# Optimization experiments

Measured on AMD Instinct MI355X. Metric: run time of the kernel, lower is better.

## Reference

```python
import jax, jax.numpy as jnp
import numpy as np

B, C, H, W = 4, 128, 64, 64
NUM_HEADS = 4
HEAD_DIM = C // NUM_HEADS


def setup_inputs() -> dict:
    key = jax.random.key(0)
    ks = jax.random.split(key, 9)
    s = 0.02
    return {
        "x": jax.random.normal(ks[0], (B, C, H, W), dtype=jnp.float32),
        "wq": jax.random.normal(ks[1], (C, C), dtype=jnp.float32) * s,
        "bq": jax.random.normal(ks[2], (C,), dtype=jnp.float32) * s,
        "wk": jax.random.normal(ks[3], (C, C), dtype=jnp.float32) * s,
        "bk": jax.random.normal(ks[4], (C,), dtype=jnp.float32) * s,
        "wv": jax.random.normal(ks[5], (C, C), dtype=jnp.float32) * s,
        "bv": jax.random.normal(ks[6], (C,), dtype=jnp.float32) * s,
        "wo": jax.random.normal(ks[7], (C, C), dtype=jnp.float32) * s,
        "bo": jax.random.normal(ks[8], (C,), dtype=jnp.float32) * s,
    }


def _proj(w, b, xf):
    # 1x1 conv == channel-mixing linear: xf is (B, C, N)
    return jnp.einsum("oc,bcn->bon", w, xf) + b[None, :, None]


def reference(x, wq, bq, wk, bk, wv, bv, wo, bo):
    b, c, h, w = x.shape
    n = h * w
    nh, hd = NUM_HEADS, HEAD_DIM
    xf = x.reshape(b, c, n)
    q = _proj(wq, bq, xf).reshape(b, nh, hd, n)
    k = _proj(wk, bk, xf).reshape(b, nh, hd, n)
    v = _proj(wv, bv, xf).reshape(b, nh, hd, n)
    # scores: (b, heads, n, n)
    scores = jnp.einsum("bhdn,bhdm->bhnm", q, k) / jnp.sqrt(jnp.float32(hd)).astype(x.dtype)
    prob = jax.nn.softmax(scores, axis=-1)
    # attn_out: (b, heads, head_dim, n)
    attn = jnp.einsum("bhnm,bhdm->bhdn", prob, v).reshape(b, c, n)
    out = _proj(wo, bo, attn).reshape(b, c, h, w)
    return x + out
```

## Files before the change

kernel.cpp:

```cpp
#include <hip/hip_runtime.h>
#include <hip/hip_bf16.h>

#define BB 4
#define CC 128
#define NN 4096
#define NHEAD 4
#define HDIM 32
#define KSPLIT 2

typedef short bf16x8_t __attribute__((ext_vector_type(8)));
typedef float f32x4_t __attribute__((ext_vector_type(4)));
typedef int i32x4_t __attribute__((ext_vector_type(4)));

#define MFMA16(a, b, c) __builtin_amdgcn_mfma_f32_16x16x32_bf16(a, b, c, 0, 0, 0)
#define EXP2(x) __builtin_amdgcn_exp2f(x)

#define QSCALE (0.17677669529663687f * 1.4426950408889634f)

static __device__ inline unsigned short f2bf(float f) {
  unsigned u = __builtin_bit_cast(unsigned, f);
  u += 0x7fffu + ((u >> 16) & 1u);
  return (unsigned short)(u >> 16);
}
static __device__ inline unsigned pack_trunc(float lo, float hi) {
  return __builtin_amdgcn_perm(__builtin_bit_cast(unsigned, hi),
                               __builtin_bit_cast(unsigned, lo), 0x07060302u);
}

static __device__ inline void gload_lds16(const unsigned short* gsrc, void* ldst) {
  __builtin_amdgcn_global_load_lds(
      (const __attribute__((address_space(1))) unsigned int*)gsrc,
      (__attribute__((address_space(3))) unsigned int*)ldst, 16, 0, 0);
}

__global__ __launch_bounds__(256) void wconv_kernel(
    const float* __restrict__ wq, const float* __restrict__ wk,
    const float* __restrict__ wv, const float* __restrict__ wo,
    unsigned short* __restrict__ wb) {
  int f = (blockIdx.x * 256 + threadIdx.x) * 8;
  int m = f >> 14, off = f & 16383;
  const float* src = (m == 0) ? wq : (m == 1) ? wk : (m == 2) ? wv : wo;
  float sc = (m == 0) ? QSCALE : 1.0f;
  float4 a = *(const float4*)(src + off);
  float4 b = *(const float4*)(src + off + 4);
  ushort4 u0, u1;
  u0.x = f2bf(a.x * sc); u0.y = f2bf(a.y * sc); u0.z = f2bf(a.z * sc); u0.w = f2bf(a.w * sc);
  u1.x = f2bf(b.x * sc); u1.y = f2bf(b.y * sc); u1.z = f2bf(b.z * sc); u1.w = f2bf(b.w * sc);
  *(ushort4*)(wb + f) = u0;
  *(ushort4*)(wb + f + 4) = u1;
}

__global__ __launch_bounds__(256) void qkv_mfma_kernel(
    const float* __restrict__ x,
    const unsigned short* __restrict__ wqb, const unsigned short* __restrict__ wkb,
    const unsigned short* __restrict__ wvb,
    const float* __restrict__ bq, const float* __restrict__ bk,
    const float* __restrict__ bv,
    unsigned short* __restrict__ qt, unsigned short* __restrict__ kt,
    unsigned short* __restrict__ vg) {
  __shared__ float xs[CC][65];
  const int b = blockIdx.y, nt = blockIdx.x, proj = blockIdx.z;
  const int tid = threadIdx.x;

#pragma unroll
  for (int i = 0; i < 8; i++) {
    int f = tid + 256 * i;
    int c = f >> 4, n4 = (f & 15) * 4;
    float4 v4 = *(const float4*)(x + ((size_t)b * CC + c) * NN + nt * 64 + n4);
    xs[c][n4 + 0] = v4.x; xs[c][n4 + 1] = v4.y;
    xs[c][n4 + 2] = v4.z; xs[c][n4 + 3] = v4.w;
  }
  __syncthreads();

  const int lane = tid & 63, w = tid >> 6;
  const int l16 = lane & 15, g = lane >> 4;
  const int nl = w * 16;

  bf16x8_t xf[4];
#pragma unroll
  for (int ks = 0; ks < 4; ks++) {
    i32x4_t pi;
#pragma unroll
    for (int p = 0; p < 4; p++) {
      float e0 = xs[ks * 32 + g * 8 + 2 * p][nl + l16];
      float e1 = xs[ks * 32 + g * 8 + 2 * p + 1][nl + l16];
      pi[p] = (int)((unsigned)f2bf(e0) | ((unsigned)f2bf(e1) << 16));
    }
    xf[ks] = __builtin_bit_cast(bf16x8_t, pi);
  }

  const int ngl = nt * 64 + nl;

  if (proj < 2) {
    const unsigned short* wm = proj ? wkb : wqb;
    const float* bias = proj ? bk : bq;
    unsigned short* dst = proj ? kt : qt;
    float bsc = proj ? 1.0f : QSCALE;
#pragma unroll
    for (int dt = 0; dt < 8; dt++) {
      float bini = bias[dt * 16 + l16] * bsc;
      f32x4_t acc = {bini, bini, bini, bini};
#pragma unroll
      for (int ks = 0; ks < 4; ks++) {
        bf16x8_t wf = *(const bf16x8_t*)(wm + (size_t)(dt * 16 + l16) * CC + ks * 32 + g * 8);
        acc = MFMA16(xf[ks], wf, acc);
      }
      int h = dt >> 1, dcol = (dt & 1) * 16 + l16;
#pragma unroll
      for (int r = 0; r < 4; r++) {
        size_t addr = (((size_t)b * NHEAD + h) * NN + (ngl + g * 4 + r)) * HDIM + dcol;
        dst[addr] = f2bf(acc[r]);
      }
    }
  } else {
    const int n = ngl + l16;
    const int mt = n >> 6, fv = (n >> 5) & 1, g2 = (n >> 2) & 3;
    const int elem = ((n >> 4) & 1) * 4 + (n & 3);
#pragma unroll
    for (int ot = 0; ot < 8; ot++) {
      f32x4_t acc;
#pragma unroll
      for (int r = 0; r < 4; r++) acc[r] = bv[ot * 16 + g * 4 + r];
#pragma unroll
      for (int ks = 0; ks < 4; ks++) {
        bf16x8_t wf = *(const bf16x8_t*)(wvb + (size_t)(ot * 16 + l16) * CC + ks * 32 + g * 8);
        acc = MFMA16(wf, xf[ks], acc);
      }
      const int hh = ot >> 1, half = ot & 1;
      const size_t base = (((size_t)(b * NHEAD + hh) * 64 + mt) * 256) * 8;
#pragma unroll
      for (int r = 0; r < 4; r++) {
        int l16v = g * 4 + r;
        size_t idx = base + (size_t)(((fv * 2 + half) * 16 + l16v) * 4 + g2) * 8 + elem;
        vg[idx] = f2bf(acc[r]);
      }
    }
  }
}

__global__ __launch_bounds__(256, 4) void attn_mfma5_kernel(
    const unsigned short* __restrict__ qt, const unsigned short* __restrict__ kt,
    const unsigned short* __restrict__ vg,
    float* __restrict__ opart, float* __restrict__ lpart) {
  __shared__ __attribute__((aligned(16))) unsigned short smem[2][4096];

  const int chunk = blockIdx.x & (KSPLIT - 1), nt = blockIdx.x / KSPLIT;
  const int h = blockIdx.y, b = blockIdx.z;
  const int bh = b * NHEAD + h;
  const int tid = threadIdx.x, lane = tid & 63, wid = tid >> 6;
  const int l16 = lane & 15, g = lane >> 4;
  const int nbase = nt * 128 + wid * 32;

  const unsigned short* qb = qt + (size_t)bh * NN * HDIM;
  const unsigned short* kb = kt + (size_t)bh * NN * HDIM;
  const unsigned short* vgb = vg + (size_t)bh * 64 * 2048;

  const bf16x8_t qf0 = *(const bf16x8_t*)(qb + (size_t)(nbase + l16) * HDIM + g * 8);
  const bf16x8_t qf1 = *(const bf16x8_t*)(qb + (size_t)(nbase + 16 + l16) * HDIM + g * 8);

  f32x4_t o00 = {0, 0, 0, 0}, o01 = {0, 0, 0, 0};
  f32x4_t o10 = {0, 0, 0, 0}, o11 = {0, 0, 0, 0};
  f32x4_t la = {0, 0, 0, 0}, lb = {0, 0, 0, 0};
  const f32x4_t zf = {0, 0, 0, 0};
  const i32x4_t onesi = {0x3F803F80, 0x3F803F80, 0x3F803F80, 0x3F803F80};
  const bf16x8_t ones = __builtin_bit_cast(bf16x8_t, onesi);

  const int NITER = 64 / KSPLIT;
  const int mt0 = chunk * NITER;

  const unsigned short* ksrc = kb + ((size_t)mt0 * 64 + wid * 16 + l16) * HDIM + g * 8;
  const unsigned short* vsrc = vgb + (size_t)mt0 * 2048 + (size_t)((wid * 16 + l16) * 4 + g) * 8;

  auto stage = [&](int p, int i) {
    gload_lds16(ksrc + (size_t)i * 2048, &smem[p][wid * 512]);
    gload_lds16(vsrc + (size_t)i * 2048, &smem[p][2048 + wid * 512]);
  };

  auto body = [&](int p) {
    const unsigned short* sk = &smem[p][0];
    bf16x8_t k0 = *(const bf16x8_t*)(sk + 0 * 512 + lane * 8);
    bf16x8_t k1 = *(const bf16x8_t*)(sk + 1 * 512 + lane * 8);
    bf16x8_t k2 = *(const bf16x8_t*)(sk + 2 * 512 + lane * 8);
    bf16x8_t k3 = *(const bf16x8_t*)(sk + 3 * 512 + lane * 8);
    bf16x8_t vf0 = *(const bf16x8_t*)(sk + 2048 + 0 * 512 + lane * 8);
    bf16x8_t vf2 = *(const bf16x8_t*)(sk + 2048 + 1 * 512 + lane * 8);
    bf16x8_t vf1 = *(const bf16x8_t*)(sk + 2048 + 2 * 512 + lane * 8);
    bf16x8_t vf3 = *(const bf16x8_t*)(sk + 2048 + 3 * 512 + lane * 8);

    f32x4_t sA0 = MFMA16(k0, qf0, zf), sA1 = MFMA16(k1, qf0, zf);
    f32x4_t sA2 = MFMA16(k2, qf0, zf), sA3 = MFMA16(k3, qf0, zf);
    f32x4_t sB0 = MFMA16(k0, qf1, zf), sB1 = MFMA16(k1, qf1, zf);
    f32x4_t sB2 = MFMA16(k2, qf1, zf), sB3 = MFMA16(k3, qf1, zf);

#pragma unroll
    for (int r = 0; r < 4; r++) {
      sA0[r] = EXP2(sA0[r]); sA1[r] = EXP2(sA1[r]);
      sA2[r] = EXP2(sA2[r]); sA3[r] = EXP2(sA3[r]);
      sB0[r] = EXP2(sB0[r]); sB1[r] = EXP2(sB1[r]);
      sB2[r] = EXP2(sB2[r]); sB3[r] = EXP2(sB3[r]);
    }

    i32x4_t pA0i = {(int)pack_trunc(sA0[0], sA0[1]), (int)pack_trunc(sA0[2], sA0[3]),
                    (int)pack_trunc(sA1[0], sA1[1]), (int)pack_trunc(sA1[2], sA1[3])};
    i32x4_t pA1i = {(int)pack_trunc(sA2[0], sA2[1]), (int)pack_trunc(sA2[2], sA2[3]),
                    (int)pack_trunc(sA3[0], sA3[1]), (int)pack_trunc(sA3[2], sA3[3])};
    i32x4_t pB0i = {(int)pack_trunc(sB0[0], sB0[1]), (int)pack_trunc(sB0[2], sB0[3]),
                    (int)pack_trunc(sB1[0], sB1[1]), (int)pack_trunc(sB1[2], sB1[3])};
    i32x4_t pB1i = {(int)pack_trunc(sB2[0], sB2[1]), (int)pack_trunc(sB2[2], sB2[3]),
                    (int)pack_trunc(sB3[0], sB3[1]), (int)pack_trunc(sB3[2], sB3[3])};
    bf16x8_t pA0 = __builtin_bit_cast(bf16x8_t, pA0i);
    bf16x8_t pA1 = __builtin_bit_cast(bf16x8_t, pA1i);
    bf16x8_t pB0 = __builtin_bit_cast(bf16x8_t, pB0i);
    bf16x8_t pB1 = __builtin_bit_cast(bf16x8_t, pB1i);

    o00 = MFMA16(vf0, pA0, o00); o00 = MFMA16(vf1, pA1, o00);
    o01 = MFMA16(vf2, pA0, o01); o01 = MFMA16(vf3, pA1, o01);
    o10 = MFMA16(vf0, pB0, o10); o10 = MFMA16(vf1, pB1, o10);
    o11 = MFMA16(vf2, pB0, o11); o11 = MFMA16(vf3, pB1, o11);

    la = MFMA16(ones, pA0, la); la = MFMA16(ones, pA1, la);
    lb = MFMA16(ones, pB0, lb); lb = MFMA16(ones, pB1, lb);
  };

  stage(0, 0);
  __syncthreads();
  for (int mi = 0; mi < NITER; mi += 2) {
    stage(1, mi + 1);
    body(0);
    __syncthreads();
    if (mi + 2 < NITER) stage(0, mi + 2);
    body(1);
    __syncthreads();
  }

  float* obase = opart + ((size_t)(chunk * BB * NHEAD + bh)) * HDIM * NN;
#pragma unroll
  for (int r = 0; r < 4; r++) {
    obase[(size_t)(g * 4 + r) * NN + nbase + l16] = o00[r];
    obase[(size_t)(16 + g * 4 + r) * NN + nbase + l16] = o01[r];
    obase[(size_t)(g * 4 + r) * NN + nbase + 16 + l16] = o10[r];
    obase[(size_t)(16 + g * 4 + r) * NN + nbase + 16 + l16] = o11[r];
  }
  if (g == 0) {
    float* lb_ = lpart + (size_t)(chunk * BB * NHEAD + bh) * NN;
    lb_[nbase + l16] = la[0];
    lb_[nbase + 16 + l16] = lb[0];
  }
}

__global__ __launch_bounds__(256) void combine_kernel(
    const float* __restrict__ opart, const float* __restrict__ lpart,
    unsigned short* __restrict__ attnT) {
  const int n = blockIdx.x * 256 + threadIdx.x;
  const int bh = blockIdx.y, dg = blockIdx.z;
  const int b = bh >> 2, h = bh & 3;

  float l = 0.f;
#pragma unroll
  for (int c = 0; c < KSPLIT; c++) l += lpart[(size_t)(c * BB * NHEAD + bh) * NN + n];
  float inv = 1.f / l;

  unsigned dw[4];
#pragma unroll
  for (int p = 0; p < 4; p++) {
    float s0 = 0.f, s1 = 0.f;
#pragma unroll
    for (int c = 0; c < KSPLIT; c++) {
      const float* ob = opart + ((size_t)(c * BB * NHEAD + bh) * HDIM + dg * 8) * NN;
      s0 += ob[(size_t)(2 * p) * NN + n];
      s1 += ob[(size_t)(2 * p + 1) * NN + n];
    }
    dw[p] = (unsigned)f2bf(s0 * inv) | ((unsigned)f2bf(s1 * inv) << 16);
  }
  unsigned short* dst = attnT + ((size_t)b * NN + n) * CC + h * HDIM + dg * 8;
  *(uint4*)dst = *(uint4*)&dw[0];
}

__global__ __launch_bounds__(256) void out_mfma_kernel(
    const unsigned short* __restrict__ attnT, const unsigned short* __restrict__ wob,
    const float* __restrict__ bo, const float* __restrict__ x,
    float* __restrict__ out) {
  const int b = blockIdx.y, nt = blockIdx.x, half = blockIdx.z;
  const int tid = threadIdx.x, lane = tid & 63, w = tid >> 6;
  const int l16 = lane & 15, g = lane >> 4;
  const int n0 = nt * 64 + w * 16;

  bf16x8_t bf[4];
#pragma unroll
  for (int ks = 0; ks < 4; ks++)
    bf[ks] = *(const bf16x8_t*)(attnT + ((size_t)b * NN + n0 + l16) * CC + ks * 32 + g * 8);

#pragma unroll
  for (int mi = 0; mi < 4; mi++) {
    int mt = half * 4 + mi;
    f32x4_t acc;
#pragma unroll
    for (int r = 0; r < 4; r++) acc[r] = bo[mt * 16 + g * 4 + r];
#pragma unroll
    for (int ks = 0; ks < 4; ks++) {
      bf16x8_t af = *(const bf16x8_t*)(wob + (size_t)(mt * 16 + l16) * CC + ks * 32 + g * 8);
      acc = MFMA16(af, bf[ks], acc);
    }
#pragma unroll
    for (int r = 0; r < 4; r++) {
      int o = mt * 16 + g * 4 + r;
      size_t addr = ((size_t)b * CC + o) * NN + n0 + l16;
      out[addr] = acc[r] + x[addr];
    }
  }
}

extern "C" void kernel_launch(void* const* d_in, const int* in_sizes, int n_in,
                              void* d_out, int out_size, void* d_ws, size_t ws_size,
                              hipStream_t stream) {
  const float* x  = (const float*)d_in[0];
  const float* wq = (const float*)d_in[1];
  const float* bq = (const float*)d_in[2];
  const float* wk = (const float*)d_in[3];
  const float* bk = (const float*)d_in[4];
  const float* wv = (const float*)d_in[5];
  const float* bv = (const float*)d_in[6];
  const float* wo = (const float*)d_in[7];
  const float* bo = (const float*)d_in[8];
  float* out = (float*)d_out;

  char* w = (char*)d_ws;
  const size_t SZ = (size_t)BB * NHEAD * NN * HDIM * 2;
  unsigned short* qt    = (unsigned short*)w;
  unsigned short* kt    = (unsigned short*)(w + SZ);
  unsigned short* vg    = (unsigned short*)(w + 2 * SZ);
  unsigned short* wb    = (unsigned short*)(w + 3 * SZ);
  float* opart = (float*)(w + 3 * SZ + 131072);
  float* lpart = (float*)(w + 3 * SZ + 131072 +
                          (size_t)KSPLIT * BB * NHEAD * HDIM * NN * 4);
  unsigned short* attnT = qt;
  unsigned short* wqb = wb, *wkb = wb + 16384, *wvb = wb + 32768, *wob = wb + 49152;

  wconv_kernel<<<32, 256, 0, stream>>>(wq, wk, wv, wo, wb);
  qkv_mfma_kernel<<<dim3(NN / 64, BB, 3), 256, 0, stream>>>(
      x, wqb, wkb, wvb, bq, bk, bv, qt, kt, vg);
  attn_mfma5_kernel<<<dim3((NN / 128) * KSPLIT, NHEAD, BB), 256, 0, stream>>>(
      qt, kt, vg, opart, lpart);
  combine_kernel<<<dim3(NN / 256, BB * NHEAD, 4), 256, 0, stream>>>(opart, lpart, attnT);
  out_mfma_kernel<<<dim3(NN / 64, BB, 2), 256, 0, stream>>>(attnT, wob, bo, x, out);
}
```

Measured before the change: 150.4 us.

## Convert x to bf16 transposed in LDS, change Q/K to d-block layout, vectorize stores

The QKV projection now converts x to bf16 while staging it into a transposed LDS tile, so MFMA fragments load as single 16-byte reads. Q and K are stored in a [d-block][n][8] layout with packed 16-byte stores made using a lane shuffle. V is staged through LDS so its swizzled layout can be written with vector stores, replacing scattered 2-byte writes. The attention kernel's Q/K addressing is updated to the new layout, and the output projection is split into quarters to launch more blocks. The extra LDS staging and barrier add some overhead to the V path.

```diff
diff --git a/kernel.cpp b/kernel.cpp
--- a/kernel.cpp
+++ b/kernel.cpp
@@ -21,6 +21,9 @@
   unsigned u = __builtin_bit_cast(unsigned, f);
   u += 0x7fffu + ((u >> 16) & 1u);
   return (unsigned short)(u >> 16);
+}
+static __device__ inline unsigned pk2(float lo, float hi) {
+  return (unsigned)f2bf(lo) | ((unsigned)f2bf(hi) << 16);
 }
 static __device__ inline unsigned pack_trunc(float lo, float hi) {
   return __builtin_amdgcn_perm(__builtin_bit_cast(unsigned, hi),
@@ -58,7 +61,8 @@
     const float* __restrict__ bv,
     unsigned short* __restrict__ qt, unsigned short* __restrict__ kt,
     unsigned short* __restrict__ vg) {
-  __shared__ float xs[CC][65];
+  __shared__ __attribute__((aligned(16))) unsigned short xsb[64][136];
+  __shared__ unsigned short vt[128][66];
   const int b = blockIdx.y, nt = blockIdx.x, proj = blockIdx.z;
   const int tid = threadIdx.x;
 
@@ -67,73 +71,72 @@
     int f = tid + 256 * i;
     int c = f >> 4, n4 = (f & 15) * 4;
     float4 v4 = *(const float4*)(x + ((size_t)b * CC + c) * NN + nt * 64 + n4);
-    xs[c][n4 + 0] = v4.x; xs[c][n4 + 1] = v4.y;
-    xs[c][n4 + 2] = v4.z; xs[c][n4 + 3] = v4.w;
+    xsb[n4 + 0][c] = f2bf(v4.x);
+    xsb[n4 + 1][c] = f2bf(v4.y);
+    xsb[n4 + 2][c] = f2bf(v4.z);
+    xsb[n4 + 3][c] = f2bf(v4.w);
   }
   __syncthreads();
 
   const int lane = tid & 63, w = tid >> 6;
   const int l16 = lane & 15, g = lane >> 4;
   const int nl = w * 16;
+  const int ngl = nt * 64 + nl;
 
   bf16x8_t xf[4];
 #pragma unroll
-  for (int ks = 0; ks < 4; ks++) {
-    i32x4_t pi;
-#pragma unroll
-    for (int p = 0; p < 4; p++) {
-      float e0 = xs[ks * 32 + g * 8 + 2 * p][nl + l16];
-      float e1 = xs[ks * 32 + g * 8 + 2 * p + 1][nl + l16];
-      pi[p] = (int)((unsigned)f2bf(e0) | ((unsigned)f2bf(e1) << 16));
-    }
-    xf[ks] = __builtin_bit_cast(bf16x8_t, pi);
-  }
-
-  const int ngl = nt * 64 + nl;
-
-  if (proj < 2) {
-    const unsigned short* wm = proj ? wkb : wqb;
-    const float* bias = proj ? bk : bq;
-    unsigned short* dst = proj ? kt : qt;
-    float bsc = proj ? 1.0f : QSCALE;
-#pragma unroll
-    for (int dt = 0; dt < 8; dt++) {
-      float bini = bias[dt * 16 + l16] * bsc;
-      f32x4_t acc = {bini, bini, bini, bini};
-#pragma unroll
-      for (int ks = 0; ks < 4; ks++) {
-        bf16x8_t wf = *(const bf16x8_t*)(wm + (size_t)(dt * 16 + l16) * CC + ks * 32 + g * 8);
-        acc = MFMA16(xf[ks], wf, acc);
+  for (int ks = 0; ks < 4; ks++)
+    xf[ks] = *(const bf16x8_t*)&xsb[nl + l16][ks * 32 + g * 8];
+
+  const unsigned short* wm = (proj == 0) ? wqb : (proj == 1) ? wkb : wvb;
+  const float* bias = (proj == 0) ? bq : (proj == 1) ? bk : bv;
+  const float bsc = (proj == 0) ? QSCALE : 1.0f;
+  unsigned short* qkdst = proj ? kt : qt;
+
+#pragma unroll
+  for (int ot = 0; ot < 8; ot++) {
+    f32x4_t acc;
+#pragma unroll
+    for (int r = 0; r < 4; r++) acc[r] = bias[ot * 16 + g * 4 + r] * bsc;
+#pragma unroll
+    for (int ks = 0; ks < 4; ks++) {
+      bf16x8_t wf = *(const bf16x8_t*)(wm + (size_t)(ot * 16 + l16) * CC + ks * 32 + g * 8);
+      acc = MFMA16(wf, xf[ks], acc);
+    }
+    if (proj < 2) {
+      unsigned p0 = pk2(acc[0], acc[1]);
+      unsigned p1 = pk2(acc[2], acc[3]);
+      unsigned q0 = (unsigned)__shfl_xor((int)p0, 16);
+      unsigned q1 = (unsigned)__shfl_xor((int)p1, 16);
+      if ((g & 1) == 0) {
+        int hh = ot >> 1, dblk = (ot & 1) * 2 + (g >> 1);
+        unsigned short* dst =
+            qkdst + (((size_t)(b * NHEAD + hh) * 4 + dblk) * NN + ngl + l16) * 8;
+        uint4 val = make_uint4(p0, p1, q0, q1);
+        *(uint4*)dst = val;
       }
-      int h = dt >> 1, dcol = (dt & 1) * 16 + l16;
-#pragma unroll
-      for (int r = 0; r < 4; r++) {
-        size_t addr = (((size_t)b * NHEAD + h) * NN + (ngl + g * 4 + r)) * HDIM + dcol;
-        dst[addr] = f2bf(acc[r]);
-      }
-    }
-  } else {
-    const int n = ngl + l16;
-    const int mt = n >> 6, fv = (n >> 5) & 1, g2 = (n >> 2) & 3;
-    const int elem = ((n >> 4) & 1) * 4 + (n & 3);
-#pragma unroll
-    for (int ot = 0; ot < 8; ot++) {
-      f32x4_t acc;
-#pragma unroll
-      for (int r = 0; r < 4; r++) acc[r] = bv[ot * 16 + g * 4 + r];
-#pragma unroll
-      for (int ks = 0; ks < 4; ks++) {
-        bf16x8_t wf = *(const bf16x8_t*)(wvb + (size_t)(ot * 16 + l16) * CC + ks * 32 + g * 8);
-        acc = MFMA16(wf, xf[ks], acc);
-      }
-      const int hh = ot >> 1, half = ot & 1;
-      const size_t base = (((size_t)(b * NHEAD + hh) * 64 + mt) * 256) * 8;
-#pragma unroll
-      for (int r = 0; r < 4; r++) {
-        int l16v = g * 4 + r;
-        size_t idx = base + (size_t)(((fv * 2 + half) * 16 + l16v) * 4 + g2) * 8 + elem;
-        vg[idx] = f2bf(acc[r]);
-      }
+    } else {
+#pragma unroll
+      for (int r = 0; r < 4; r++) vt[ot * 16 + g * 4 + r][nl + l16] = f2bf(acc[r]);
+    }
+  }
+
+  if (proj == 2) {
+    __syncthreads();
+#pragma unroll
+    for (int c = 0; c < 4; c++) {
+      int cid = c * 256 + tid;
+      int hh = cid >> 8, inner = cid & 255;
+      int g2 = inner & 3, l16v = (inner >> 2) & 15, fh = inner >> 6;
+      int fv = fh >> 1, half = fh & 1;
+      int o = hh * 32 + half * 16 + l16v;
+      int n0 = fv * 32 + g2 * 4;
+      unsigned d0 = *(const unsigned*)&vt[o][n0];
+      unsigned d1 = *(const unsigned*)&vt[o][n0 + 2];
+      unsigned d2 = *(const unsigned*)&vt[o][n0 + 16];
+      unsigned d3 = *(const unsigned*)&vt[o][n0 + 18];
+      uint4 val = make_uint4(d0, d1, d2, d3);
+      *(uint4*)(vg + (((size_t)(b * NHEAD + hh) * 64 + nt) * 256 + inner) * 8) = val;
     }
   }
 }
@@ -155,8 +158,8 @@
   const unsigned short* kb = kt + (size_t)bh * NN * HDIM;
   const unsigned short* vgb = vg + (size_t)bh * 64 * 2048;
 
-  const bf16x8_t qf0 = *(const bf16x8_t*)(qb + (size_t)(nbase + l16) * HDIM + g * 8);
-  const bf16x8_t qf1 = *(const bf16x8_t*)(qb + (size_t)(nbase + 16 + l16) * HDIM + g * 8);
+  const bf16x8_t qf0 = *(const bf16x8_t*)(qb + ((size_t)g * NN + nbase + l16) * 8);
+  const bf16x8_t qf1 = *(const bf16x8_t*)(qb + ((size_t)g * NN + nbase + 16 + l16) * 8);
 
   f32x4_t o00 = {0, 0, 0, 0}, o01 = {0, 0, 0, 0};
   f32x4_t o10 = {0, 0, 0, 0}, o11 = {0, 0, 0, 0};
@@ -168,11 +171,11 @@
   const int NITER = 64 / KSPLIT;
   const int mt0 = chunk * NITER;
 
-  const unsigned short* ksrc = kb + ((size_t)mt0 * 64 + wid * 16 + l16) * HDIM + g * 8;
+  const unsigned short* ksrc = kb + ((size_t)g * NN + mt0 * 64 + wid * 16 + l16) * 8;
   const unsigned short* vsrc = vgb + (size_t)mt0 * 2048 + (size_t)((wid * 16 + l16) * 4 + g) * 8;
 
   auto stage = [&](int p, int i) {
-    gload_lds16(ksrc + (size_t)i * 2048, &smem[p][wid * 512]);
+    gload_lds16(ksrc + (size_t)i * 512, &smem[p][wid * 512]);
     gload_lds16(vsrc + (size_t)i * 2048, &smem[p][2048 + wid * 512]);
   };
 
@@ -280,7 +283,7 @@
     const unsigned short* __restrict__ attnT, const unsigned short* __restrict__ wob,
     const float* __restrict__ bo, const float* __restrict__ x,
     float* __restrict__ out) {
-  const int b = blockIdx.y, nt = blockIdx.x, half = blockIdx.z;
+  const int b = blockIdx.y, nt = blockIdx.x, quarter = blockIdx.z;
   const int tid = threadIdx.x, lane = tid & 63, w = tid >> 6;
   const int l16 = lane & 15, g = lane >> 4;
   const int n0 = nt * 64 + w * 16;
@@ -291,8 +294,8 @@
     bf[ks] = *(const bf16x8_t*)(attnT + ((size_t)b * NN + n0 + l16) * CC + ks * 32 + g * 8);
 
 #pragma unroll
-  for (int mi = 0; mi < 4; mi++) {
-    int mt = half * 4 + mi;
+  for (int mi = 0; mi < 2; mi++) {
+    int mt = quarter * 2 + mi;
     f32x4_t acc;
 #pragma unroll
     for (int r = 0; r < 4; r++) acc[r] = bo[mt * 16 + g * 4 + r];
@@ -342,5 +345,5 @@
   attn_mfma5_kernel<<<dim3((NN / 128) * KSPLIT, NHEAD, BB), 256, 0, stream>>>(
       qt, kt, vg, opart, lpart);
   combine_kernel<<<dim3(NN / 256, BB * NHEAD, 4), 256, 0, stream>>>(opart, lpart, attnT);
-  out_mfma_kernel<<<dim3(NN / 64, BB, 2), 256, 0, stream>>>(attnT, wob, bo, x, out);
-}
+  out_mfma_kernel<<<dim3(NN / 64, BB, 4), 256, 0, stream>>>(attnT, wob, bo, x, out);
+}
```

Result: no change. 148.4 us (-1.3%).
